# Kernel optimization log

Hardware: AMD Instinct MI355X
Metric: run time of the kernel (lower is better)

## Reference

```python
import jax, jax.numpy as jnp
import numpy as np

D_MODEL = 1024
N_HEADS = 16
HEAD_DIM = D_MODEL // N_HEADS


def apply_rope(x):
    # x: [B, S, H, Dh]; standard rotate-half RoPE over head_dim
    B, S, H, Dh = x.shape
    inv_freq = 1.0 / (10000.0 ** (jnp.arange(0, Dh, 2, dtype=jnp.float32) / Dh))  # [Dh/2]
    pos = jnp.arange(S, dtype=jnp.float32)
    freqs = pos[:, None] * inv_freq[None, :]          # [S, Dh/2]
    cos = jnp.cos(freqs)[None, :, None, :]            # [1, S, 1, Dh/2]
    sin = jnp.sin(freqs)[None, :, None, :]
    x1, x2 = x[..., :Dh // 2], x[..., Dh // 2:]
    return jnp.concatenate([x1 * cos - x2 * sin, x1 * sin + x2 * cos], axis=-1)


def setup_inputs() -> dict:
    key = jax.random.key(0)
    ks = jax.random.split(key, 8)
    B, S, D = 2, 2048, D_MODEL
    s = 0.02
    return {
        "query": jax.random.normal(ks[0], (B, S, D), dtype=jnp.float32),
        "key": jax.random.normal(ks[1], (B, S, D), dtype=jnp.float32),
        "value": jax.random.normal(ks[2], (B, S, D), dtype=jnp.float32),
        "Wq": jax.random.normal(ks[3], (D, D), dtype=jnp.float32) * s,
        "Wk": jax.random.normal(ks[4], (D, D), dtype=jnp.float32) * s,
        "Wv": jax.random.normal(ks[5], (D, D), dtype=jnp.float32) * s,
        "Wo": jax.random.normal(ks[6], (D, D), dtype=jnp.float32) * s,
        "bo": jax.random.normal(ks[7], (D,), dtype=jnp.float32) * s,
    }


def reference(query, key, value, Wq, Wk, Wv, Wo, bo):
    B, Sq, D = query.shape
    Skv = key.shape[1]
    H, Dh = N_HEADS, HEAD_DIM
    scale = Dh ** -0.5
    # projections (torch Linear: x @ W.T)
    q = (query @ Wq.T).reshape(B, Sq, H, Dh)
    k = (key @ Wk.T).reshape(B, Skv, H, Dh)
    v = (value @ Wv.T).reshape(B, Skv, H, Dh)
    q = apply_rope(q)
    k = apply_rope(k)
    # scores: [B, H, Sq, Skv]
    scores = jnp.einsum("bqhd,bkhd->bhqk", q, k) * scale
    attn_weights = jax.nn.softmax(scores, axis=-1)
    out = jnp.einsum("bhqk,bkhd->bqhd", attn_weights, v).reshape(B, Sq, D)
    out = out @ Wo.T + bo
    return out, attn_weights
```

## Files before the change

### kernel.cpp

```cpp
#include <hip/hip_runtime.h>
#include <math.h>

#define D_MODEL 1024
#define SEQ     2048
#define NB      2
#define NH      16
#define DH      64
#define ROWS    (NB*SEQ)
#define OUT_ELEMS ((size_t)ROWS*D_MODEL)

typedef short bf16x8 __attribute__((ext_vector_type(8)));
typedef short bf16x4 __attribute__((ext_vector_type(4)));
typedef float f32x4  __attribute__((ext_vector_type(4)));

#define AS1 __attribute__((address_space(1)))
#define AS3 __attribute__((address_space(3)))

__device__ __forceinline__ float bf2f(short u){
    union{float f; unsigned v;} x; x.v = ((unsigned)(unsigned short)u) << 16; return x.f;
}
__device__ __forceinline__ short f2bf(float f){
    union{float f; unsigned v;} x; x.f = f;
    unsigned r = (x.v + 0x7FFF + ((x.v >> 16) & 1)) >> 16;
    return (short)r;
}
__device__ __forceinline__ int swz8(int row, int slot){ return slot ^ ((row + (row>>3)) & 7); }

#define MFMA16(a,b,c) __builtin_amdgcn_mfma_f32_16x16x32_bf16((a),(b),(c),0,0,0)

#define EXPSC 0.18033688011112042f

__global__ __launch_bounds__(256) void prep(const float* __restrict__ Wq,
                                            const float* __restrict__ Wk,
                                            const float* __restrict__ Wv,
                                            const float* __restrict__ Wo,
                                            short* __restrict__ wqkv,
                                            short* __restrict__ wob,
                                            float* __restrict__ tab)
{
    int i = blockIdx.x*256 + threadIdx.x;
    if (i < 1048576) {
        int sel = i >> 18;
        int loc = i & 262143;
        const float* src = sel==0 ? Wq : sel==1 ? Wk : sel==2 ? Wv : Wo;
        short* dst = sel < 3 ? wqkv + (size_t)sel*1048576 : wob;
        float4 v = *(const float4*)&src[(size_t)loc*4];
        bf16x4 o = { f2bf(v.x), f2bf(v.y), f2bf(v.z), f2bf(v.w) };
        *(bf16x4*)&dst[(size_t)loc*4] = o;
    } else {
        int e = i - 1048576;
        int j = e & 31, s = e >> 5;
        float ang = (float)s * exp2f(-(float)j * 0.41524101186092437f);
        float sn, cs; sincosf(ang, &sn, &cs);
        tab[(size_t)s*64 + j*2]     = cs;
        tab[(size_t)s*64 + j*2 + 1] = sn;
    }
}

__global__ __launch_bounds__(256) void gemm_qkv(const float* __restrict__ qx,
                                                const float* __restrict__ kx,
                                                const float* __restrict__ vx,
                                                const short* __restrict__ wqkv,
                                                const float* __restrict__ tab,
                                                short* __restrict__ qb,
                                                short* __restrict__ kb,
                                                short* __restrict__ vbt)
{
    const int z = blockIdx.z;
    const float* A = z==0 ? qx : z==1 ? kx : vx;
    const short* B = wqkv + (size_t)z*D_MODEL*D_MODEL;

    __shared__ __align__(16) short Alds[128*32];
    __shared__ __align__(16) short Blds[128*32];
    const int t = threadIdx.x, lane = t & 63, wid = t >> 6;
    const int m0 = blockIdx.y << 7, n0 = blockIdx.x << 7;
    const int wm = (wid >> 1) << 6, wn = (wid & 1) << 6;
    const int l15 = lane & 15, l4 = lane >> 4;

    f32x4 acc[4][4] = {};

    for (int k0 = 0; k0 < D_MODEL; k0 += 32) {
        float4 ar[4];
        #pragma unroll
        for (int u = 0; u < 4; ++u) {
            int id = u*256 + t;
            int row = id >> 3, c4 = id & 7;
            ar[u] = *(const float4*)&A[(size_t)(m0+row)*D_MODEL + k0 + c4*4];
        }
        __syncthreads();
        #pragma unroll
        for (int u = 0; u < 4; ++u) {
            int id = u*256 + t;
            int row = id >> 3, c4 = id & 7;
            bf16x4 a4 = { f2bf(ar[u].x), f2bf(ar[u].y), f2bf(ar[u].z), f2bf(ar[u].w) };
            *(bf16x4*)&Alds[row*32 + c4*4] = a4;
        }
        #pragma unroll
        for (int u = 0; u < 2; ++u) {
            int row = (wid*2 + u)*16 + (lane >> 2);
            int kc  = k0 + (lane & 3)*8;
            const short* gb = &B[(size_t)(n0 + row)*D_MODEL + kc];
            __builtin_amdgcn_global_load_lds((const AS1 unsigned*)gb,
                (AS3 unsigned*)&Blds[(wid*2 + u)*512], 16, 0, 0);
        }
        __syncthreads();
        bf16x8 af[4], bfr[4];
        #pragma unroll
        for (int mf = 0; mf < 4; ++mf)
            af[mf] = *(const bf16x8*)&Alds[(wm + mf*16 + l15)*32 + l4*8];
        #pragma unroll
        for (int nf = 0; nf < 4; ++nf)
            bfr[nf] = *(const bf16x8*)&Blds[(wn + nf*16 + l15)*32 + l4*8];
        #pragma unroll
        for (int mf = 0; mf < 4; ++mf)
            #pragma unroll
            for (int nf = 0; nf < 4; ++nf)
                acc[mf][nf] = MFMA16(af[mf], bfr[nf], acc[mf][nf]);
    }

    if (z < 2) {
        short* C = z==0 ? qb : kb;
        #pragma unroll
        for (int mf = 0; mf < 4; ++mf)
            #pragma unroll
            for (int j = 0; j < 4; ++j) {
                int row = m0 + wm + mf*16 + l4*4 + j;
                int s = row & (SEQ-1);
                #pragma unroll
                for (int p = 0; p < 2; ++p) {
                    int d31 = p*16 + l15;
                    float2 cs2 = *(const float2*)&tab[(size_t)s*64 + d31*2];
                    float x1 = acc[mf][p][j], x2 = acc[mf][p+2][j];
                    size_t rb = (size_t)row*D_MODEL + n0 + wn;
                    C[rb + p*16 + l15]       = f2bf(x1*cs2.x - x2*cs2.y);
                    C[rb + (p+2)*16 + l15]   = f2bf(x1*cs2.y + x2*cs2.x);
                }
            }
    } else {
        #pragma unroll
        for (int nf = 0; nf < 4; ++nf) {
            int col = n0 + wn + nf*16 + l15;
            int hh = col >> 6, d = col & 63;
            #pragma unroll
            for (int mf = 0; mf < 4; ++mf)
                #pragma unroll
                for (int j = 0; j < 4; ++j) {
                    int row = m0 + wm + mf*16 + l4*4 + j;
                    int b = row >> 11, s = row & (SEQ-1);
                    vbt[(((size_t)(b*NH + hh))*DH + d)*SEQ + s] = f2bf(acc[mf][nf][j]);
                }
        }
    }
}

__global__ __launch_bounds__(256) void gemm_out(const short* __restrict__ A,
                                                const short* __restrict__ B,
                                                const float* __restrict__ bias,
                                                float* __restrict__ Cout)
{
    __shared__ __align__(16) short Alds[128*32];
    __shared__ __align__(16) short Blds[128*32];
    const int t = threadIdx.x, lane = t & 63, wid = t >> 6;
    const int m0 = blockIdx.y << 7, n0 = blockIdx.x << 7;
    const int wm = (wid >> 1) << 6, wn = (wid & 1) << 6;
    const int l15 = lane & 15, l4 = lane >> 4;

    f32x4 acc[4][4] = {};

    for (int k0 = 0; k0 < D_MODEL; k0 += 32) {
        __syncthreads();
        #pragma unroll
        for (int u = 0; u < 2; ++u) {
            int row = (wid*2 + u)*16 + (lane >> 2);
            int kc  = k0 + (lane & 3)*8;
            const short* ga = &A[(size_t)(m0 + row)*D_MODEL + kc];
            const short* gb = &B[(size_t)(n0 + row)*D_MODEL + kc];
            __builtin_amdgcn_global_load_lds((const AS1 unsigned*)ga,
                (AS3 unsigned*)&Alds[(wid*2 + u)*512], 16, 0, 0);
            __builtin_amdgcn_global_load_lds((const AS1 unsigned*)gb,
                (AS3 unsigned*)&Blds[(wid*2 + u)*512], 16, 0, 0);
        }
        __syncthreads();
        bf16x8 af[4], bfr[4];
        #pragma unroll
        for (int mf = 0; mf < 4; ++mf)
            af[mf] = *(const bf16x8*)&Alds[(wm + mf*16 + l15)*32 + l4*8];
        #pragma unroll
        for (int nf = 0; nf < 4; ++nf)
            bfr[nf] = *(const bf16x8*)&Blds[(wn + nf*16 + l15)*32 + l4*8];
        #pragma unroll
        for (int mf = 0; mf < 4; ++mf)
            #pragma unroll
            for (int nf = 0; nf < 4; ++nf)
                acc[mf][nf] = MFMA16(af[mf], bfr[nf], acc[mf][nf]);
    }

    #pragma unroll
    for (int nf = 0; nf < 4; ++nf) {
        int col = n0 + wn + nf*16 + l15;
        float bv = bias[col];
        #pragma unroll
        for (int mf = 0; mf < 4; ++mf)
            #pragma unroll
            for (int j = 0; j < 4; ++j) {
                int row = m0 + wm + mf*16 + l4*4 + j;
                Cout[(size_t)row*D_MODEL + col] = acc[mf][nf][j] + bv;
            }
    }
}

__global__ __launch_bounds__(512) void attn_fused(const short* __restrict__ qb,
                                                  const short* __restrict__ kb,
                                                  const short* __restrict__ vbt,
                                                  float* __restrict__ attn,
                                                  short* __restrict__ aob)
{
    __shared__ __align__(16) short Klds[64*64];
    __shared__ __align__(16) short Vt  [64*64];
    __shared__ __align__(16) short Plds[8*16*64];
    const int t = threadIdx.x, lane = t & 63, wv = t >> 6;
    const int bid = blockIdx.x;
    const int nb = (bid & 7)*64 + (bid >> 3);
    const int rb = nb & 15, bh = nb >> 4;
    const int h = bh & 15;
    const size_t bs0 = (size_t)(bh >> 4) * SEQ;
    const int qrow0 = rb << 7;
    const int l15 = lane & 15, l4 = lane >> 4;
    const int srow = t >> 3, ssl = t & 7;

    bf16x8 qf[2];
    {
        int qrow = qrow0 + wv*16 + l15;
        const short* qp = &qb[(bs0 + qrow)*D_MODEL + h*DH + l4*8];
        qf[0] = *(const bf16x8*)&qp[0];
        qf[1] = *(const bf16x8*)&qp[32];
    }

    const short* kbase  = &kb[(bs0 + srow)*D_MODEL + h*DH + ssl*8];
    const short* vtbase = &vbt[((size_t)bh*DH + srow)*SEQ + ssl*8];

    float lsum = 0.f;
    bf16x8 kreg = *(const bf16x8*)&kbase[0];
    for (int kt = 0; kt < SEQ; kt += 64) {
        __syncthreads();
        *(bf16x8*)&Klds[srow*64 + swz8(srow, ssl)*8] = kreg;
        __syncthreads();
        if (kt + 64 < SEQ)
            kreg = *(const bf16x8*)&kbase[(size_t)(kt+64)*D_MODEL];
        f32x4 sc[4] = {};
        __builtin_amdgcn_s_setprio(1);
        #pragma unroll
        for (int kk = 0; kk < 2; ++kk)
            #pragma unroll
            for (int nf = 0; nf < 4; ++nf) {
                int krow = nf*16 + l15;
                bf16x8 kf = *(const bf16x8*)&Klds[krow*64 + swz8(krow, kk*4 + l4)*8];
                sc[nf] = MFMA16(kf, qf[kk], sc[nf]);
            }
        __builtin_amdgcn_s_setprio(0);
        #pragma unroll
        for (int nf = 0; nf < 4; ++nf)
            #pragma unroll
            for (int j = 0; j < 4; ++j)
                lsum += exp2f(sc[nf][j]*EXPSC);
    }
    lsum += __shfl_xor(lsum, 16);
    lsum += __shfl_xor(lsum, 32);
    const float li = 1.0f / lsum;

    f32x4 o[4] = {};
    kreg = *(const bf16x8*)&kbase[0];
    bf16x8 vreg = *(const bf16x8*)&vtbase[0];
    const size_t wrow = ((size_t)bh*SEQ + qrow0 + wv*16 + l15)*SEQ;
    short* pbase = &Plds[wv*1024 + l15*64];
    for (int kt = 0; kt < SEQ; kt += 64) {
        __syncthreads();
        *(bf16x8*)&Klds[srow*64 + swz8(srow, ssl)*8] = kreg;
        *(bf16x8*)&Vt  [srow*64 + swz8(srow, ssl)*8] = vreg;
        __syncthreads();
        if (kt + 64 < SEQ) {
            kreg = *(const bf16x8*)&kbase[(size_t)(kt+64)*D_MODEL];
            vreg = *(const bf16x8*)&vtbase[kt+64];
        }
        f32x4 sc[4] = {};
        __builtin_amdgcn_s_setprio(1);
        #pragma unroll
        for (int kk = 0; kk < 2; ++kk)
            #pragma unroll
            for (int nf = 0; nf < 4; ++nf) {
                int krow = nf*16 + l15;
                bf16x8 kf = *(const bf16x8*)&Klds[krow*64 + swz8(krow, kk*4 + l4)*8];
                sc[nf] = MFMA16(kf, qf[kk], sc[nf]);
            }
        __builtin_amdgcn_s_setprio(0);
        #pragma unroll
        for (int nf = 0; nf < 4; ++nf) {
            float w0 = exp2f(sc[nf][0]*EXPSC) * li;
            float w1 = exp2f(sc[nf][1]*EXPSC) * li;
            float w2 = exp2f(sc[nf][2]*EXPSC) * li;
            float w3 = exp2f(sc[nf][3]*EXPSC) * li;
            f32x4 wv4 = { w0, w1, w2, w3 };
            __builtin_nontemporal_store(wv4,
                (f32x4*)&attn[wrow + kt + nf*16 + l4*4]);
            bf16x4 pw = { f2bf(w0), f2bf(w1), f2bf(w2), f2bf(w3) };
            *(bf16x4*)&pbase[swz8(l15, nf*2 + (l4>>1))*8 + (l4&1)*4] = pw;
        }
        __builtin_amdgcn_s_setprio(1);
        #pragma unroll
        for (int kk = 0; kk < 2; ++kk) {
            bf16x8 pa = *(const bf16x8*)&pbase[swz8(l15, kk*4 + l4)*8];
            #pragma unroll
            for (int nf = 0; nf < 4; ++nf) {
                int d = nf*16 + l15;
                bf16x8 vf = *(const bf16x8*)&Vt[d*64 + swz8(d, kk*4 + l4)*8];
                o[nf] = MFMA16(pa, vf, o[nf]);
            }
        }
        __builtin_amdgcn_s_setprio(0);
    }
    #pragma unroll
    for (int nf = 0; nf < 4; ++nf)
        #pragma unroll
        for (int j = 0; j < 4; ++j) {
            int qr = qrow0 + wv*16 + l4*4 + j;
            aob[(bs0 + qr)*D_MODEL + h*DH + nf*16 + l15] = f2bf(o[nf][j]);
        }
}

extern "C" void kernel_launch(void* const* d_in, const int* in_sizes, int n_in,
                              void* d_out, int out_size, void* d_ws, size_t ws_size,
                              hipStream_t stream)
{
    const float* query = (const float*)d_in[0];
    const float* key_  = (const float*)d_in[1];
    const float* value = (const float*)d_in[2];
    const float* Wq    = (const float*)d_in[3];
    const float* Wk    = (const float*)d_in[4];
    const float* Wv    = (const float*)d_in[5];
    const float* Wo    = (const float*)d_in[6];
    const float* bo    = (const float*)d_in[7];

    float* out  = (float*)d_out;
    float* attn = out + OUT_ELEMS;

    short* wqkv = (short*)d_ws;
    short* wob  = wqkv + (size_t)3*1048576;
    short* qb   = wob  + (size_t)1048576;
    short* kb   = qb + OUT_ELEMS;
    short* vbt  = kb + OUT_ELEMS;
    short* aob  = vbt + OUT_ELEMS;
    float* tab  = (float*)(aob + OUT_ELEMS);

    dim3 blk(256);

    hipLaunchKernelGGL(prep, dim3(4352), blk, 0, stream, Wq, Wk, Wv, Wo, wqkv, wob, tab);
    hipLaunchKernelGGL(gemm_qkv, dim3(8, 32, 3), blk, 0, stream,
                       query, key_, value, wqkv, tab, qb, kb, vbt);
    hipLaunchKernelGGL(attn_fused, dim3(512), dim3(512), 0, stream,
                       qb, kb, vbt, attn, aob);
    hipLaunchKernelGGL(gemm_out, dim3(8, 32), blk, 0, stream, aob, wob, bo, out);
}
```

Before: 316.8 us.

## Pre-convert activations to bf16 and double-buffer K/V tiles in attention

The prep kernel now converts query/key/value to bf16 into scratch space inside the attn output buffer, so gemm_qkv shares gemm_out's global_load_lds path for both operands and no longer converts fp32 in registers. The attention kernel double-buffers the K and V LDS tiles, writing the next tile while computing on the current one and dropping one barrier per iteration. The cost is an extra pass over the activations (fp32 read plus bf16 write) and twice the K/V LDS footprint. It also relies on attn_fused fully overwriting the attn buffer after gemm_qkv has consumed the scratch.

```diff
diff --git a/kernel.cpp b/kernel.cpp
--- a/kernel.cpp
+++ b/kernel.cpp
@@ -34,8 +34,12 @@
                                             const float* __restrict__ Wk,
                                             const float* __restrict__ Wv,
                                             const float* __restrict__ Wo,
+                                            const float* __restrict__ qx,
+                                            const float* __restrict__ kx,
+                                            const float* __restrict__ vx,
                                             short* __restrict__ wqkv,
                                             short* __restrict__ wob,
+                                            short* __restrict__ xb,
                                             float* __restrict__ tab)
 {
     int i = blockIdx.x*256 + threadIdx.x;
@@ -47,8 +51,17 @@
         float4 v = *(const float4*)&src[(size_t)loc*4];
         bf16x4 o = { f2bf(v.x), f2bf(v.y), f2bf(v.z), f2bf(v.w) };
         *(bf16x4*)&dst[(size_t)loc*4] = o;
+    } else if (i < 4194304) {
+        int e = i - 1048576;
+        int sel = e >> 20;
+        int loc = e & 1048575;
+        const float* src = sel==0 ? qx : sel==1 ? kx : vx;
+        short* dst = xb + (size_t)sel*OUT_ELEMS;
+        float4 v = *(const float4*)&src[(size_t)loc*4];
+        bf16x4 o = { f2bf(v.x), f2bf(v.y), f2bf(v.z), f2bf(v.w) };
+        *(bf16x4*)&dst[(size_t)loc*4] = o;
     } else {
-        int e = i - 1048576;
+        int e = i - 4194304;
         int j = e & 31, s = e >> 5;
         float ang = (float)s * exp2f(-(float)j * 0.41524101186092437f);
         float sn, cs; sincosf(ang, &sn, &cs);
@@ -57,9 +70,7 @@
     }
 }
 
-__global__ __launch_bounds__(256) void gemm_qkv(const float* __restrict__ qx,
-                                                const float* __restrict__ kx,
-                                                const float* __restrict__ vx,
+__global__ __launch_bounds__(256) void gemm_qkv(const short* __restrict__ xb,
                                                 const short* __restrict__ wqkv,
                                                 const float* __restrict__ tab,
                                                 short* __restrict__ qb,
@@ -67,97 +78,9 @@
                                                 short* __restrict__ vbt)
 {
     const int z = blockIdx.z;
-    const float* A = z==0 ? qx : z==1 ? kx : vx;
+    const short* A = xb + (size_t)z*OUT_ELEMS;
     const short* B = wqkv + (size_t)z*D_MODEL*D_MODEL;
 
-    __shared__ __align__(16) short Alds[128*32];
-    __shared__ __align__(16) short Blds[128*32];
-    const int t = threadIdx.x, lane = t & 63, wid = t >> 6;
-    const int m0 = blockIdx.y << 7, n0 = blockIdx.x << 7;
-    const int wm = (wid >> 1) << 6, wn = (wid & 1) << 6;
-    const int l15 = lane & 15, l4 = lane >> 4;
-
-    f32x4 acc[4][4] = {};
-
-    for (int k0 = 0; k0 < D_MODEL; k0 += 32) {
-        float4 ar[4];
-        #pragma unroll
-        for (int u = 0; u < 4; ++u) {
-            int id = u*256 + t;
-            int row = id >> 3, c4 = id & 7;
-            ar[u] = *(const float4*)&A[(size_t)(m0+row)*D_MODEL + k0 + c4*4];
-        }
-        __syncthreads();
-        #pragma unroll
-        for (int u = 0; u < 4; ++u) {
-            int id = u*256 + t;
-            int row = id >> 3, c4 = id & 7;
-            bf16x4 a4 = { f2bf(ar[u].x), f2bf(ar[u].y), f2bf(ar[u].z), f2bf(ar[u].w) };
-            *(bf16x4*)&Alds[row*32 + c4*4] = a4;
-        }
-        #pragma unroll
-        for (int u = 0; u < 2; ++u) {
-            int row = (wid*2 + u)*16 + (lane >> 2);
-            int kc  = k0 + (lane & 3)*8;
-            const short* gb = &B[(size_t)(n0 + row)*D_MODEL + kc];
-            __builtin_amdgcn_global_load_lds((const AS1 unsigned*)gb,
-                (AS3 unsigned*)&Blds[(wid*2 + u)*512], 16, 0, 0);
-        }
-        __syncthreads();
-        bf16x8 af[4], bfr[4];
-        #pragma unroll
-        for (int mf = 0; mf < 4; ++mf)
-            af[mf] = *(const bf16x8*)&Alds[(wm + mf*16 + l15)*32 + l4*8];
-        #pragma unroll
-        for (int nf = 0; nf < 4; ++nf)
-            bfr[nf] = *(const bf16x8*)&Blds[(wn + nf*16 + l15)*32 + l4*8];
-        #pragma unroll
-        for (int mf = 0; mf < 4; ++mf)
-            #pragma unroll
-            for (int nf = 0; nf < 4; ++nf)
-                acc[mf][nf] = MFMA16(af[mf], bfr[nf], acc[mf][nf]);
-    }
-
-    if (z < 2) {
-        short* C = z==0 ? qb : kb;
-        #pragma unroll
-        for (int mf = 0; mf < 4; ++mf)
-            #pragma unroll
-            for (int j = 0; j < 4; ++j) {
-                int row = m0 + wm + mf*16 + l4*4 + j;
-                int s = row & (SEQ-1);
-                #pragma unroll
-                for (int p = 0; p < 2; ++p) {
-                    int d31 = p*16 + l15;
-                    float2 cs2 = *(const float2*)&tab[(size_t)s*64 + d31*2];
-                    float x1 = acc[mf][p][j], x2 = acc[mf][p+2][j];
-                    size_t rb = (size_t)row*D_MODEL + n0 + wn;
-                    C[rb + p*16 + l15]       = f2bf(x1*cs2.x - x2*cs2.y);
-                    C[rb + (p+2)*16 + l15]   = f2bf(x1*cs2.y + x2*cs2.x);
-                }
-            }
-    } else {
-        #pragma unroll
-        for (int nf = 0; nf < 4; ++nf) {
-            int col = n0 + wn + nf*16 + l15;
-            int hh = col >> 6, d = col & 63;
-            #pragma unroll
-            for (int mf = 0; mf < 4; ++mf)
-                #pragma unroll
-                for (int j = 0; j < 4; ++j) {
-                    int row = m0 + wm + mf*16 + l4*4 + j;
-                    int b = row >> 11, s = row & (SEQ-1);
-                    vbt[(((size_t)(b*NH + hh))*DH + d)*SEQ + s] = f2bf(acc[mf][nf][j]);
-                }
-        }
-    }
-}
-
-__global__ __launch_bounds__(256) void gemm_out(const short* __restrict__ A,
-                                                const short* __restrict__ B,
-                                                const float* __restrict__ bias,
-                                                float* __restrict__ Cout)
-{
     __shared__ __align__(16) short Alds[128*32];
     __shared__ __align__(16) short Blds[128*32];
     const int t = threadIdx.x, lane = t & 63, wid = t >> 6;
@@ -195,6 +118,83 @@
                 acc[mf][nf] = MFMA16(af[mf], bfr[nf], acc[mf][nf]);
     }
 
+    if (z < 2) {
+        short* C = z==0 ? qb : kb;
+        #pragma unroll
+        for (int mf = 0; mf < 4; ++mf)
+            #pragma unroll
+            for (int j = 0; j < 4; ++j) {
+                int row = m0 + wm + mf*16 + l4*4 + j;
+                int s = row & (SEQ-1);
+                #pragma unroll
+                for (int p = 0; p < 2; ++p) {
+                    int d31 = p*16 + l15;
+                    float2 cs2 = *(const float2*)&tab[(size_t)s*64 + d31*2];
+                    float x1 = acc[mf][p][j], x2 = acc[mf][p+2][j];
+                    size_t rb = (size_t)row*D_MODEL + n0 + wn;
+                    C[rb + p*16 + l15]       = f2bf(x1*cs2.x - x2*cs2.y);
+                    C[rb + (p+2)*16 + l15]   = f2bf(x1*cs2.y + x2*cs2.x);
+                }
+            }
+    } else {
+        #pragma unroll
+        for (int nf = 0; nf < 4; ++nf) {
+            int col = n0 + wn + nf*16 + l15;
+            int hh = col >> 6, d = col & 63;
+            #pragma unroll
+            for (int mf = 0; mf < 4; ++mf)
+                #pragma unroll
+                for (int j = 0; j < 4; ++j) {
+                    int row = m0 + wm + mf*16 + l4*4 + j;
+                    int b = row >> 11, s = row & (SEQ-1);
+                    vbt[(((size_t)(b*NH + hh))*DH + d)*SEQ + s] = f2bf(acc[mf][nf][j]);
+                }
+        }
+    }
+}
+
+__global__ __launch_bounds__(256) void gemm_out(const short* __restrict__ A,
+                                                const short* __restrict__ B,
+                                                const float* __restrict__ bias,
+                                                float* __restrict__ Cout)
+{
+    __shared__ __align__(16) short Alds[128*32];
+    __shared__ __align__(16) short Blds[128*32];
+    const int t = threadIdx.x, lane = t & 63, wid = t >> 6;
+    const int m0 = blockIdx.y << 7, n0 = blockIdx.x << 7;
+    const int wm = (wid >> 1) << 6, wn = (wid & 1) << 6;
+    const int l15 = lane & 15, l4 = lane >> 4;
+
+    f32x4 acc[4][4] = {};
+
+    for (int k0 = 0; k0 < D_MODEL; k0 += 32) {
+        __syncthreads();
+        #pragma unroll
+        for (int u = 0; u < 2; ++u) {
+            int row = (wid*2 + u)*16 + (lane >> 2);
+            int kc  = k0 + (lane & 3)*8;
+            const short* ga = &A[(size_t)(m0 + row)*D_MODEL + kc];
+            const short* gb = &B[(size_t)(n0 + row)*D_MODEL + kc];
+            __builtin_amdgcn_global_load_lds((const AS1 unsigned*)ga,
+                (AS3 unsigned*)&Alds[(wid*2 + u)*512], 16, 0, 0);
+            __builtin_amdgcn_global_load_lds((const AS1 unsigned*)gb,
+                (AS3 unsigned*)&Blds[(wid*2 + u)*512], 16, 0, 0);
+        }
+        __syncthreads();
+        bf16x8 af[4], bfr[4];
+        #pragma unroll
+        for (int mf = 0; mf < 4; ++mf)
+            af[mf] = *(const bf16x8*)&Alds[(wm + mf*16 + l15)*32 + l4*8];
+        #pragma unroll
+        for (int nf = 0; nf < 4; ++nf)
+            bfr[nf] = *(const bf16x8*)&Blds[(wn + nf*16 + l15)*32 + l4*8];
+        #pragma unroll
+        for (int mf = 0; mf < 4; ++mf)
+            #pragma unroll
+            for (int nf = 0; nf < 4; ++nf)
+                acc[mf][nf] = MFMA16(af[mf], bfr[nf], acc[mf][nf]);
+    }
+
     #pragma unroll
     for (int nf = 0; nf < 4; ++nf) {
         int col = n0 + wn + nf*16 + l15;
@@ -215,8 +215,8 @@
                                                   float* __restrict__ attn,
                                                   short* __restrict__ aob)
 {
-    __shared__ __align__(16) short Klds[64*64];
-    __shared__ __align__(16) short Vt  [64*64];
+    __shared__ __align__(16) short Klds[2][64*64];
+    __shared__ __align__(16) short Vt  [2][64*64];
     __shared__ __align__(16) short Plds[8*16*64];
     const int t = threadIdx.x, lane = t & 63, wv = t >> 6;
     const int bid = blockIdx.x;
@@ -227,6 +227,7 @@
     const int qrow0 = rb << 7;
     const int l15 = lane & 15, l4 = lane >> 4;
     const int srow = t >> 3, ssl = t & 7;
+    const int soff = srow*64 + swz8(srow, ssl)*8;
 
     bf16x8 qf[2];
     {
@@ -240,83 +241,99 @@
     const short* vtbase = &vbt[((size_t)bh*DH + srow)*SEQ + ssl*8];
 
     float lsum = 0.f;
-    bf16x8 kreg = *(const bf16x8*)&kbase[0];
-    for (int kt = 0; kt < SEQ; kt += 64) {
-        __syncthreads();
-        *(bf16x8*)&Klds[srow*64 + swz8(srow, ssl)*8] = kreg;
-        __syncthreads();
-        if (kt + 64 < SEQ)
-            kreg = *(const bf16x8*)&kbase[(size_t)(kt+64)*D_MODEL];
-        f32x4 sc[4] = {};
-        __builtin_amdgcn_s_setprio(1);
-        #pragma unroll
-        for (int kk = 0; kk < 2; ++kk)
-            #pragma unroll
-            for (int nf = 0; nf < 4; ++nf) {
-                int krow = nf*16 + l15;
-                bf16x8 kf = *(const bf16x8*)&Klds[krow*64 + swz8(krow, kk*4 + l4)*8];
-                sc[nf] = MFMA16(kf, qf[kk], sc[nf]);
-            }
-        __builtin_amdgcn_s_setprio(0);
-        #pragma unroll
-        for (int nf = 0; nf < 4; ++nf)
-            #pragma unroll
-            for (int j = 0; j < 4; ++j)
-                lsum += exp2f(sc[nf][j]*EXPSC);
+    {
+        bf16x8 kreg = *(const bf16x8*)&kbase[0];
+        *(bf16x8*)&Klds[0][soff] = kreg;
+        kreg = *(const bf16x8*)&kbase[(size_t)64*D_MODEL];
+        __syncthreads();
+        int cur = 0;
+        for (int kt = 0; kt < SEQ; kt += 64, cur ^= 1) {
+            if (kt + 64 < SEQ) {
+                *(bf16x8*)&Klds[cur^1][soff] = kreg;
+                if (kt + 128 < SEQ)
+                    kreg = *(const bf16x8*)&kbase[(size_t)(kt+128)*D_MODEL];
+            }
+            f32x4 sc[4] = {};
+            __builtin_amdgcn_s_setprio(1);
+            #pragma unroll
+            for (int kk = 0; kk < 2; ++kk)
+                #pragma unroll
+                for (int nf = 0; nf < 4; ++nf) {
+                    int krow = nf*16 + l15;
+                    bf16x8 kf = *(const bf16x8*)&Klds[cur][krow*64 + swz8(krow, kk*4 + l4)*8];
+                    sc[nf] = MFMA16(kf, qf[kk], sc[nf]);
+                }
+            __builtin_amdgcn_s_setprio(0);
+            #pragma unroll
+            for (int nf = 0; nf < 4; ++nf)
+                #pragma unroll
+                for (int j = 0; j < 4; ++j)
+                    lsum += exp2f(sc[nf][j]*EXPSC);
+            __syncthreads();
+        }
     }
     lsum += __shfl_xor(lsum, 16);
     lsum += __shfl_xor(lsum, 32);
     const float li = 1.0f / lsum;
 
     f32x4 o[4] = {};
-    kreg = *(const bf16x8*)&kbase[0];
-    bf16x8 vreg = *(const bf16x8*)&vtbase[0];
     const size_t wrow = ((size_t)bh*SEQ + qrow0 + wv*16 + l15)*SEQ;
     short* pbase = &Plds[wv*1024 + l15*64];
-    for (int kt = 0; kt < SEQ; kt += 64) {
-        __syncthreads();
-        *(bf16x8*)&Klds[srow*64 + swz8(srow, ssl)*8] = kreg;
-        *(bf16x8*)&Vt  [srow*64 + swz8(srow, ssl)*8] = vreg;
-        __syncthreads();
-        if (kt + 64 < SEQ) {
-            kreg = *(const bf16x8*)&kbase[(size_t)(kt+64)*D_MODEL];
-            vreg = *(const bf16x8*)&vtbase[kt+64];
-        }
-        f32x4 sc[4] = {};
-        __builtin_amdgcn_s_setprio(1);
-        #pragma unroll
-        for (int kk = 0; kk < 2; ++kk)
+    {
+        bf16x8 kreg = *(const bf16x8*)&kbase[0];
+        bf16x8 vreg = *(const bf16x8*)&vtbase[0];
+        *(bf16x8*)&Klds[0][soff] = kreg;
+        *(bf16x8*)&Vt  [0][soff] = vreg;
+        kreg = *(const bf16x8*)&kbase[(size_t)64*D_MODEL];
+        vreg = *(const bf16x8*)&vtbase[64];
+        __syncthreads();
+        int cur = 0;
+        for (int kt = 0; kt < SEQ; kt += 64, cur ^= 1) {
+            if (kt + 64 < SEQ) {
+                *(bf16x8*)&Klds[cur^1][soff] = kreg;
+                *(bf16x8*)&Vt  [cur^1][soff] = vreg;
+                if (kt + 128 < SEQ) {
+                    kreg = *(const bf16x8*)&kbase[(size_t)(kt+128)*D_MODEL];
+                    vreg = *(const bf16x8*)&vtbase[kt+128];
+                }
+            }
+            f32x4 sc[4] = {};
+            __builtin_amdgcn_s_setprio(1);
+            #pragma unroll
+            for (int kk = 0; kk < 2; ++kk)
+                #pragma unroll
+                for (int nf = 0; nf < 4; ++nf) {
+                    int krow = nf*16 + l15;
+                    bf16x8 kf = *(const bf16x8*)&Klds[cur][krow*64 + swz8(krow, kk*4 + l4)*8];
+                    sc[nf] = MFMA16(kf, qf[kk], sc[nf]);
+                }
+            __builtin_amdgcn_s_setprio(0);
             #pragma unroll
             for (int nf = 0; nf < 4; ++nf) {
-                int krow = nf*16 + l15;
-                bf16x8 kf = *(const bf16x8*)&Klds[krow*64 + swz8(krow, kk*4 + l4)*8];
-                sc[nf] = MFMA16(kf, qf[kk], sc[nf]);
-            }
-        __builtin_amdgcn_s_setprio(0);
-        #pragma unroll
-        for (int nf = 0; nf < 4; ++nf) {
-            float w0 = exp2f(sc[nf][0]*EXPSC) * li;
-            float w1 = exp2f(sc[nf][1]*EXPSC) * li;
-            float w2 = exp2f(sc[nf][2]*EXPSC) * li;
-            float w3 = exp2f(sc[nf][3]*EXPSC) * li;
-            f32x4 wv4 = { w0, w1, w2, w3 };
-            __builtin_nontemporal_store(wv4,
-                (f32x4*)&attn[wrow + kt + nf*16 + l4*4]);
-            bf16x4 pw = { f2bf(w0), f2bf(w1), f2bf(w2), f2bf(w3) };
-            *(bf16x4*)&pbase[swz8(l15, nf*2 + (l4>>1))*8 + (l4&1)*4] = pw;
-        }
-        __builtin_amdgcn_s_setprio(1);
-        #pragma unroll
-        for (int kk = 0; kk < 2; ++kk) {
-            bf16x8 pa = *(const bf16x8*)&pbase[swz8(l15, kk*4 + l4)*8];
-            #pragma unroll
-            for (int nf = 0; nf < 4; ++nf) {
-                int d = nf*16 + l15;
-                bf16x8 vf = *(const bf16x8*)&Vt[d*64 + swz8(d, kk*4 + l4)*8];
-                o[nf] = MFMA16(pa, vf, o[nf]);
-            }
-        }
-        __builtin_amdgcn_s_setprio(0);
+                float w0 = exp2f(sc[nf][0]*EXPSC) * li;
+                float w1 = exp2f(sc[nf][1]*EXPSC) * li;
+                float w2 = exp2f(sc[nf][2]*EXPSC) * li;
+                float w3 = exp2f(sc[nf][3]*EXPSC) * li;
+                f32x4 wv4 = { w0, w1, w2, w3 };
+                __builtin_nontemporal_store(wv4,
+                    (f32x4*)&attn[wrow + kt + nf*16 + l4*4]);
+                bf16x4 pw = { f2bf(w0), f2bf(w1), f2bf(w2), f2bf(w3) };
+                *(bf16x4*)&pbase[swz8(l15, nf*2 + (l4>>1))*8 + (l4&1)*4] = pw;
+            }
+            __builtin_amdgcn_s_setprio(1);
+            #pragma unroll
+            for (int kk = 0; kk < 2; ++kk) {
+                bf16x8 pa = *(const bf16x8*)&pbase[swz8(l15, kk*4 + l4)*8];
+                #pragma unroll
+                for (int nf = 0; nf < 4; ++nf) {
+                    int d = nf*16 + l15;
+                    bf16x8 vf = *(const bf16x8*)&Vt[cur][d*64 + swz8(d, kk*4 + l4)*8];
+                    o[nf] = MFMA16(pa, vf, o[nf]);
+                }
+            }
+            __builtin_amdgcn_s_setprio(0);
+            __syncthreads();
+        }
     }
     #pragma unroll
     for (int nf = 0; nf < 4; ++nf)
@@ -342,6 +359,7 @@
 
     float* out  = (float*)d_out;
     float* attn = out + OUT_ELEMS;
+    short* xb   = (short*)attn;
 
     short* wqkv = (short*)d_ws;
     short* wob  = wqkv + (size_t)3*1048576;
@@ -353,9 +371,10 @@
 
     dim3 blk(256);
 
-    hipLaunchKernelGGL(prep, dim3(4352), blk, 0, stream, Wq, Wk, Wv, Wo, wqkv, wob, tab);
+    hipLaunchKernelGGL(prep, dim3(16640), blk, 0, stream,
+                       Wq, Wk, Wv, Wo, query, key_, value, wqkv, wob, xb, tab);
     hipLaunchKernelGGL(gemm_qkv, dim3(8, 32, 3), blk, 0, stream,
-                       query, key_, value, wqkv, tab, qb, kb, vbt);
+                       xb, wqkv, tab, qb, kb, vbt);
     hipLaunchKernelGGL(attn_fused, dim3(512), dim3(512), 0, stream,
                        qb, kb, vbt, attn, aob);
     hipLaunchKernelGGL(gemm_out, dim3(8, 32), blk, 0, stream, aob, wob, bo, out);
```

Measured after the change: 296.6 us. 6.4% less time.
